# Performance work log

Measured on AMD Instinct MI355X. Metric: run time of the kernel, lower is better.

Reference implementation:

```python
import jax, jax.numpy as jnp
import numpy as np

EPS = 1e-12  # F.normalize eps


def sage_conv(x, src, dst, n_nodes, W_l, b_l, W_r):
    """PyG SAGEConv with mean aggregation and L2 normalize.
    out = lin_l(mean_{j in N(i)} x_j) + lin_r(x_i), then row-wise L2 normalize.
    """
    # mean-aggregate neighbor features: scatter-add then divide by in-degree
    msg_sum = jax.ops.segment_sum(x[src], dst, num_segments=n_nodes)  # [N, F]
    deg = jax.ops.segment_sum(jnp.ones_like(dst, dtype=x.dtype), dst,
                              num_segments=n_nodes)                   # [N]
    agg = msg_sum / jnp.maximum(deg, 1.0)[:, None]
    out = agg @ W_l + b_l + x @ W_r                                   # [N, out]
    norm = jnp.sqrt(jnp.sum(out * out, axis=-1, keepdims=True))
    return out / jnp.maximum(norm, EPS)


def setup_inputs() -> dict:
    key = jax.random.key(0)
    ks = jax.random.split(key, 8)
    N, E, D_IN, D_H, D_OUT = 100000, 320000, 256, 64, 4
    x = jax.random.normal(ks[0], (N, D_IN), dtype=jnp.float32)
    edge_index = jax.random.randint(ks[1], (2, E), 0, N, dtype=jnp.int32)
    s1 = 1.0 / np.sqrt(D_IN)
    s2 = 1.0 / np.sqrt(D_H)
    W1_l = jax.random.uniform(ks[2], (D_IN, D_H), jnp.float32, -s1, s1)
    b1_l = jnp.zeros((D_H,), jnp.float32)
    W1_r = jax.random.uniform(ks[3], (D_IN, D_H), jnp.float32, -s1, s1)
    W2_l = jax.random.uniform(ks[4], (D_H, D_OUT), jnp.float32, -s2, s2)
    b2_l = jnp.zeros((D_OUT,), jnp.float32)
    W2_r = jax.random.uniform(ks[5], (D_H, D_OUT), jnp.float32, -s2, s2)
    return {"x": x, "edge_index": edge_index,
            "W1_l": W1_l, "b1_l": b1_l, "W1_r": W1_r,
            "W2_l": W2_l, "b2_l": b2_l, "W2_r": W2_r}


def reference(x, edge_index, W1_l, b1_l, W1_r, W2_l, b2_l, W2_r):
    # eval mode: dropout is identity
    n_nodes = x.shape[0]
    src, dst = edge_index[0], edge_index[1]
    h = jax.nn.relu(sage_conv(x, src, dst, n_nodes, W1_l, b1_l, W1_r))
    out = sage_conv(h, src, dst, n_nodes, W2_l, b2_l, W2_r)
    return out
```

## Files before the change

### kernel.cpp

```cpp
#include <hip/hip_runtime.h>

#define DIN 256
#define DH  64
#define DOUT 4

typedef __attribute__((ext_vector_type(8))) short bf16x8;
typedef __attribute__((ext_vector_type(4))) float f32x4;

__device__ __forceinline__ short f2bf(float f) {
    unsigned int u = __float_as_uint(f);
    unsigned int r = (u + 0x7FFFu + ((u >> 16) & 1u)) >> 16;
    return (short)r;
}
__device__ __forceinline__ short f2bf_trunc(float f) {
    return (short)(__float_as_uint(f) >> 16);
}
__device__ __forceinline__ float bf2f(short h) {
    return __uint_as_float(((unsigned int)(unsigned short)h) << 16);
}

__global__ void count_kernel(const int* __restrict__ dst, int* __restrict__ cnt, int E) {
    int e = blockIdx.x * blockDim.x + threadIdx.x;
    if (e < E) atomicAdd(&cnt[dst[e]], 1);
}

__global__ void scan_a_kernel(const int* __restrict__ cnt, int* __restrict__ blocksum, int N) {
    __shared__ int s[256];
    const int t = threadIdx.x;
    const int gi = blockIdx.x * 256 + t;
    s[t] = (gi < N) ? cnt[gi] : 0;
    __syncthreads();
    for (int stp = 128; stp > 0; stp >>= 1) {
        if (t < stp) s[t] += s[t + stp];
        __syncthreads();
    }
    if (t == 0) blocksum[blockIdx.x] = s[0];
}

__global__ void scan_b_kernel(int* __restrict__ blocksum, int* __restrict__ blockoff, int nblk) {
    __shared__ int s[1024];
    const int t = threadIdx.x;
    int v = (t < nblk) ? blocksum[t] : 0;
    s[t] = v;
    __syncthreads();
    for (int stp = 1; stp < 1024; stp <<= 1) {
        int add = (t >= stp) ? s[t - stp] : 0;
        __syncthreads();
        s[t] += add;
        __syncthreads();
    }
    if (t < nblk) blockoff[t] = s[t] - v;
}

__global__ void scan_c_kernel(const int* __restrict__ cnt, const int* __restrict__ blockoff,
                              int* __restrict__ off, int N) {
    __shared__ int s[256];
    const int t = threadIdx.x;
    const int gi = blockIdx.x * 256 + t;
    int v = (gi < N) ? cnt[gi] : 0;
    s[t] = v;
    __syncthreads();
    for (int stp = 1; stp < 256; stp <<= 1) {
        int add = (t >= stp) ? s[t - stp] : 0;
        __syncthreads();
        s[t] += add;
        __syncthreads();
    }
    if (gi <= N) off[gi] = blockoff[blockIdx.x] + s[t] - v;
}

__global__ void fill_kernel(const int* __restrict__ src, const int* __restrict__ dst,
                            const int* __restrict__ off, int* __restrict__ cursor,
                            int* __restrict__ nbr, int E) {
    int e = blockIdx.x * blockDim.x + threadIdx.x;
    if (e >= E) return;
    const int d = dst[e];
    const int p = atomicAdd(&cursor[d], 1);
    nbr[off[d] + p] = src[e];
}

__global__ void wprep_kernel(const float* __restrict__ Wl, const float* __restrict__ Wr,
                             short* __restrict__ WTh, short* __restrict__ WTl) {
    const int k = threadIdx.x;
    const int n = blockIdx.x;
    const float v = (n < 64) ? Wl[k * 64 + n] : Wr[k * 64 + (n - 64)];
    const short hi = f2bf(v);
    const short lo = f2bf(v - bf2f(hi));
    WTh[n * 256 + k] = hi;
    WTl[n * 256 + k] = lo;
}

#define XS_LD 40
__global__ __launch_bounds__(256, 4) void gemm1_mfma(
    const float* __restrict__ x, const short* __restrict__ WTh,
    const short* __restrict__ WTl, float* __restrict__ y, int N)
{
    __shared__ short xsh[2][64 * XS_LD];
    __shared__ short xsl[2][64 * XS_LD];

    const int tid  = threadIdx.x;
    const int wave = tid >> 6;
    const int lane = tid & 63;
    const int lm   = lane & 15;
    const int quad = lane >> 4;
    const int brow = blockIdx.x * 64;

    const int xr    = tid >> 2;
    const int xk    = (tid & 3) * 8;
    const int row_g = brow + xr;
    const bool xvalid = (row_g < N);
    const float* xptr = x + (size_t)row_g * DIN + xk;
    const int xs_off = xr * XS_LD + xk;

    const int col0 = wave * 32 + lm;
    const size_t wb0 = (size_t)col0 * 256 + quad * 8;
    const size_t wb1 = (size_t)(col0 + 16) * 256 + quad * 8;

    f32x4 acc[4][2];
    #pragma unroll
    for (int mt = 0; mt < 4; ++mt)
        #pragma unroll
        for (int nt = 0; nt < 2; ++nt)
            acc[mt][nt] = (f32x4){0.f, 0.f, 0.f, 0.f};

    {
        float4 a, b;
        if (xvalid) {
            a = ((const float4*)xptr)[0];
            b = ((const float4*)xptr)[1];
        } else {
            a = b = make_float4(0.f, 0.f, 0.f, 0.f);
        }
        bf16x8 ph, pl;
        float fv[8] = {a.x, a.y, a.z, a.w, b.x, b.y, b.z, b.w};
        #pragma unroll
        for (int j = 0; j < 8; ++j) {
            const short hi = f2bf_trunc(fv[j]);
            ph[j] = hi;
            pl[j] = f2bf_trunc(fv[j] - bf2f(hi));
        }
        *(bf16x8*)(&xsh[0][xs_off]) = ph;
        *(bf16x8*)(&xsl[0][xs_off]) = pl;
    }
    bf16x8 wh_cur[2], wl_cur[2];
    wh_cur[0] = *(const bf16x8*)(WTh + wb0);
    wh_cur[1] = *(const bf16x8*)(WTh + wb1);
    wl_cur[0] = *(const bf16x8*)(WTl + wb0);
    wl_cur[1] = *(const bf16x8*)(WTl + wb1);
    __syncthreads();

    #pragma unroll
    for (int k = 0; k < 8; ++k) {
        const int buf = k & 1;

        float4 na, nb;
        bf16x8 wh_nxt[2], wl_nxt[2];
        if (k < 7) {
            const int kc = (k + 1) * 32;
            if (xvalid) {
                na = ((const float4*)(xptr + kc))[0];
                nb = ((const float4*)(xptr + kc))[1];
            } else {
                na = nb = make_float4(0.f, 0.f, 0.f, 0.f);
            }
            wh_nxt[0] = *(const bf16x8*)(WTh + wb0 + kc);
            wh_nxt[1] = *(const bf16x8*)(WTh + wb1 + kc);
            wl_nxt[0] = *(const bf16x8*)(WTl + wb0 + kc);
            wl_nxt[1] = *(const bf16x8*)(WTl + wb1 + kc);
        }

        #pragma unroll
        for (int mt = 0; mt < 4; ++mt) {
            const int aoff = (mt * 16 + lm) * XS_LD + quad * 8;
            const bf16x8 ah = *(const bf16x8*)(&xsh[buf][aoff]);
            const bf16x8 al = *(const bf16x8*)(&xsl[buf][aoff]);
            #pragma unroll
            for (int nt = 0; nt < 2; ++nt) {
                acc[mt][nt] = __builtin_amdgcn_mfma_f32_16x16x32_bf16(
                    ah, wh_cur[nt], acc[mt][nt], 0, 0, 0);
                acc[mt][nt] = __builtin_amdgcn_mfma_f32_16x16x32_bf16(
                    ah, wl_cur[nt], acc[mt][nt], 0, 0, 0);
                acc[mt][nt] = __builtin_amdgcn_mfma_f32_16x16x32_bf16(
                    al, wh_cur[nt], acc[mt][nt], 0, 0, 0);
            }
        }

        if (k < 7) {
            bf16x8 ph, pl;
            float fv[8] = {na.x, na.y, na.z, na.w, nb.x, nb.y, nb.z, nb.w};
            #pragma unroll
            for (int j = 0; j < 8; ++j) {
                const short hi = f2bf_trunc(fv[j]);
                ph[j] = hi;
                pl[j] = f2bf_trunc(fv[j] - bf2f(hi));
            }
            *(bf16x8*)(&xsh[buf ^ 1][xs_off]) = ph;
            *(bf16x8*)(&xsl[buf ^ 1][xs_off]) = pl;
            #pragma unroll
            for (int nt = 0; nt < 2; ++nt) {
                wh_cur[nt] = wh_nxt[nt];
                wl_cur[nt] = wl_nxt[nt];
            }
            __syncthreads();
        }
    }

    #pragma unroll
    for (int mt = 0; mt < 4; ++mt) {
        #pragma unroll
        for (int r = 0; r < 4; ++r) {
            const int rg = brow + mt * 16 + quad * 4 + r;
            if (rg < N) {
                const int col = wave * 32 + lm;
                float* yp = y + (size_t)rg * 128 + col;
                yp[0]  = acc[mt][0][r];
                yp[16] = acc[mt][1][r];
            }
        }
    }
}

__global__ __launch_bounds__(256) void fused1_kernel(
    const float* __restrict__ y, const int* __restrict__ off, const int* __restrict__ nbr,
    const float* __restrict__ b1, const float* __restrict__ W2l, const float* __restrict__ W2r,
    float* __restrict__ z, int N)
{
    const int wave = threadIdx.x >> 6;
    const int lane = threadIdx.x & 63;
    const int i = blockIdx.x * 4 + wave;
    if (i >= N) return;

    const int beg = off[i];
    const int end = off[i + 1];
    const int deg = end - beg;

    const int dd = (deg < 64) ? deg : 64;
    int myn = (lane < dd) ? nbr[beg + lane] : 0;

    float acc = 0.f;
    int j = 0;
    for (; j + 1 < dd; j += 2) {
        const int s0 = __shfl(myn, j, 64);
        const int s1 = __shfl(myn, j + 1, 64);
        const float v0 = y[(size_t)s0 * 128 + lane];
        const float v1 = y[(size_t)s1 * 128 + lane];
        acc += v0 + v1;
    }
    if (j < dd) {
        const int s0 = __shfl(myn, j, 64);
        acc += y[(size_t)s0 * 128 + lane];
    }
    for (int q = beg + 64; q < end; ++q) {
        const int s = nbr[q];
        acc += y[(size_t)s * 128 + lane];
    }

    const float dinv = 1.0f / fmaxf((float)deg, 1.0f);
    float v = acc * dinv + b1[lane] + y[(size_t)i * 128 + 64 + lane];

    float ss = v * v;
    #pragma unroll
    for (int m = 32; m >= 1; m >>= 1) ss += __shfl_xor(ss, m, 64);
    const float inv = 1.0f / fmaxf(sqrtf(ss), 1e-12f);
    const float hv = fmaxf(v * inv, 0.f);

    const float4 wl = *(const float4*)(W2l + lane * 4);
    const float4 wr = *(const float4*)(W2r + lane * 4);
    float p0 = hv * wl.x, p1 = hv * wl.y, p2 = hv * wl.z, p3 = hv * wl.w;
    float p4 = hv * wr.x, p5 = hv * wr.y, p6 = hv * wr.z, p7 = hv * wr.w;

    const bool b0 = (lane & 1) != 0;
    float s0_ = b0 ? p0 : p4;
    float s1_ = b0 ? p1 : p5;
    float s2_ = b0 ? p2 : p6;
    float s3_ = b0 ? p3 : p7;
    float q0 = (b0 ? p4 : p0) + __shfl_xor(s0_, 1, 64);
    float q1 = (b0 ? p5 : p1) + __shfl_xor(s1_, 1, 64);
    float q2 = (b0 ? p6 : p2) + __shfl_xor(s2_, 1, 64);
    float q3 = (b0 ? p7 : p3) + __shfl_xor(s3_, 1, 64);
    const bool b1b = (lane & 2) != 0;
    float t0 = b1b ? q0 : q2;
    float t1 = b1b ? q1 : q3;
    float r0 = (b1b ? q2 : q0) + __shfl_xor(t0, 2, 64);
    float r1 = (b1b ? q3 : q1) + __shfl_xor(t1, 2, 64);
    const bool b2 = (lane & 4) != 0;
    float u0 = b2 ? r0 : r1;
    float zv = (b2 ? r1 : r0) + __shfl_xor(u0, 4, 64);
    zv += __shfl_xor(zv, 8, 64);
    zv += __shfl_xor(zv, 16, 64);
    zv += __shfl_xor(zv, 32, 64);
    const int ch = 4 * (lane & 1) + ((lane & 2)) + ((lane >> 2) & 1);
    if (lane < 8) z[(size_t)i * 8 + ch] = zv;
}

__global__ void fused2_kernel(const float* __restrict__ z, const int* __restrict__ off,
                              const int* __restrict__ nbr, const float* __restrict__ b2,
                              float* __restrict__ out, int N)
{
    const int i = blockIdx.x * blockDim.x + threadIdx.x;
    if (i >= N) return;
    const int beg = off[i];
    const int end = off[i + 1];
    float4 acc = make_float4(0.f, 0.f, 0.f, 0.f);
    for (int j = beg; j < end; ++j) {
        const int s = nbr[j];
        const float4 t = *(const float4*)(z + (size_t)s * 8);
        acc.x += t.x; acc.y += t.y; acc.z += t.z; acc.w += t.w;
    }
    const float dinv = 1.0f / fmaxf((float)(end - beg), 1.0f);
    const float4 r  = *(const float4*)(z + (size_t)i * 8 + 4);
    const float4 bb = *(const float4*)(b2);
    float4 o;
    o.x = acc.x * dinv + bb.x + r.x;
    o.y = acc.y * dinv + bb.y + r.y;
    o.z = acc.z * dinv + bb.z + r.z;
    o.w = acc.w * dinv + bb.w + r.w;
    const float ss = o.x * o.x + o.y * o.y + o.z * o.z + o.w * o.w;
    const float inv = 1.0f / fmaxf(sqrtf(ss), 1e-12f);
    o.x *= inv; o.y *= inv; o.z *= inv; o.w *= inv;
    *(float4*)(out + (size_t)i * 4) = o;
}

extern "C" void kernel_launch(void* const* d_in, const int* in_sizes, int n_in,
                              void* d_out, int out_size, void* d_ws, size_t ws_size,
                              hipStream_t stream)
{
    const float* x    = (const float*)d_in[0];
    const int*   ei   = (const int*)d_in[1];
    const float* W1l  = (const float*)d_in[2];
    const float* b1l  = (const float*)d_in[3];
    const float* W1r  = (const float*)d_in[4];
    const float* W2l  = (const float*)d_in[5];
    const float* b2l  = (const float*)d_in[6];
    const float* W2r  = (const float*)d_in[7];
    float* out = (float*)d_out;

    const int N = in_sizes[0] / DIN;
    const int E = in_sizes[1] / 2;
    const int* src = ei;
    const int* dst = ei + E;
    const int nblk = (N + 255) / 256;

    char* ws = (char*)d_ws;
    size_t woff = 0;
    auto alloc = [&](size_t bytes) {
        void* p = ws + woff;
        woff += (bytes + 255) & ~(size_t)255;
        return p;
    };
    float* y        = (float*)alloc((size_t)N * 128 * 4);
    float* z        = (float*)alloc((size_t)N * 8 * 4);
    short* WTh      = (short*)alloc((size_t)128 * 256 * 2);
    short* WTl      = (short*)alloc((size_t)128 * 256 * 2);
    int*   cnt      = (int*)alloc((size_t)2 * N * 4);
    int*   cursor   = cnt + N;
    int*   off      = (int*)alloc((size_t)(N + 1) * 4);
    int*   nbr      = (int*)alloc((size_t)E * 4);
    int*   blocksum = (int*)alloc((size_t)nblk * 4);
    int*   blockoff = (int*)alloc((size_t)nblk * 4);

    hipMemsetAsync(cnt, 0, (size_t)2 * N * 4, stream);

    count_kernel<<<(E + 255) / 256, 256, 0, stream>>>(dst, cnt, E);
    scan_a_kernel<<<nblk, 256, 0, stream>>>(cnt, blocksum, N);
    scan_b_kernel<<<1, 1024, 0, stream>>>(blocksum, blockoff, nblk);
    scan_c_kernel<<<nblk, 256, 0, stream>>>(cnt, blockoff, off, N);
    fill_kernel<<<(E + 255) / 256, 256, 0, stream>>>(src, dst, off, cursor, nbr, E);

    wprep_kernel<<<128, 256, 0, stream>>>(W1l, W1r, WTh, WTl);
    gemm1_mfma<<<(N + 63) / 64, 256, 0, stream>>>(x, WTh, WTl, y, N);

    fused1_kernel<<<(N + 3) / 4, 256, 0, stream>>>(y, off, nbr, b1l, W2l, W2r, z, N);

    fused2_kernel<<<(N + 255) / 256, 256, 0, stream>>>(z, off, nbr, b2l, out, N);
}
```

Baseline: 273.8 us.

## Drop LDS staging in GEMM1 and reuse degree counts as fill cursor

The first-layer GEMM no longer stages x tiles through shared memory with block barriers. Each wave now loads its own 32-row strip straight into registers, splits it to bf16 hi/lo, and computes 64 output columns with a two-stage register prefetch of x and weights. This removes the LDS traffic and __syncthreads, but each x row is now read by two waves and register pressure rises, so the occupancy hint drops from 4 to 3. Separately, the CSR fill decrements the count array instead of using a second cursor array, which halves the memset size.

```diff
diff --git a/kernel.cpp b/kernel.cpp
--- a/kernel.cpp
+++ b/kernel.cpp
@@ -70,12 +70,12 @@
 }
 
 __global__ void fill_kernel(const int* __restrict__ src, const int* __restrict__ dst,
-                            const int* __restrict__ off, int* __restrict__ cursor,
+                            const int* __restrict__ off, int* __restrict__ cnt,
                             int* __restrict__ nbr, int E) {
     int e = blockIdx.x * blockDim.x + threadIdx.x;
     if (e >= E) return;
     const int d = dst[e];
-    const int p = atomicAdd(&cursor[d], 1);
+    const int p = atomicSub(&cnt[d], 1) - 1;
     nbr[off[d] + p] = src[e];
 }
 
@@ -90,131 +90,107 @@
     WTl[n * 256 + k] = lo;
 }
 
-#define XS_LD 40
-__global__ __launch_bounds__(256, 4) void gemm1_mfma(
+__global__ __launch_bounds__(256, 3) void gemm1_mfma(
     const float* __restrict__ x, const short* __restrict__ WTh,
     const short* __restrict__ WTl, float* __restrict__ y, int N)
 {
-    __shared__ short xsh[2][64 * XS_LD];
-    __shared__ short xsl[2][64 * XS_LD];
-
-    const int tid  = threadIdx.x;
-    const int wave = tid >> 6;
-    const int lane = tid & 63;
-    const int lm   = lane & 15;
-    const int quad = lane >> 4;
-    const int brow = blockIdx.x * 64;
-
-    const int xr    = tid >> 2;
-    const int xk    = (tid & 3) * 8;
-    const int row_g = brow + xr;
-    const bool xvalid = (row_g < N);
-    const float* xptr = x + (size_t)row_g * DIN + xk;
-    const int xs_off = xr * XS_LD + xk;
-
-    const int col0 = wave * 32 + lm;
-    const size_t wb0 = (size_t)col0 * 256 + quad * 8;
-    const size_t wb1 = (size_t)(col0 + 16) * 256 + quad * 8;
-
-    f32x4 acc[4][2];
-    #pragma unroll
-    for (int mt = 0; mt < 4; ++mt)
+    const int tid   = threadIdx.x;
+    const int wave  = tid >> 6;
+    const int lane  = tid & 63;
+    const int lm    = lane & 15;
+    const int quad  = lane >> 4;
+    const int strip = blockIdx.x * 2 + (wave >> 1);
+    const int ch    = wave & 1;
+    const int wrow  = strip * 32;
+    if (wrow >= N) return;
+
+    const int r0 = min(wrow + lm,      N - 1);
+    const int r1 = min(wrow + 16 + lm, N - 1);
+    const float* xp0 = x + (size_t)r0 * DIN + quad * 8;
+    const float* xp1 = x + (size_t)r1 * DIN + quad * 8;
+
+    const short* wph = WTh + (size_t)(ch * 64 + lm) * 256 + quad * 8;
+    const short* wpl = WTl + (size_t)(ch * 64 + lm) * 256 + quad * 8;
+
+    f32x4 acc[2][4];
+    #pragma unroll
+    for (int mt = 0; mt < 2; ++mt)
         #pragma unroll
-        for (int nt = 0; nt < 2; ++nt)
+        for (int nt = 0; nt < 4; ++nt)
             acc[mt][nt] = (f32x4){0.f, 0.f, 0.f, 0.f};
 
-    {
-        float4 a, b;
-        if (xvalid) {
-            a = ((const float4*)xptr)[0];
-            b = ((const float4*)xptr)[1];
-        } else {
-            a = b = make_float4(0.f, 0.f, 0.f, 0.f);
-        }
-        bf16x8 ph, pl;
-        float fv[8] = {a.x, a.y, a.z, a.w, b.x, b.y, b.z, b.w};
-        #pragma unroll
-        for (int j = 0; j < 8; ++j) {
-            const short hi = f2bf_trunc(fv[j]);
-            ph[j] = hi;
-            pl[j] = f2bf_trunc(fv[j] - bf2f(hi));
-        }
-        *(bf16x8*)(&xsh[0][xs_off]) = ph;
-        *(bf16x8*)(&xsl[0][xs_off]) = pl;
-    }
-    bf16x8 wh_cur[2], wl_cur[2];
-    wh_cur[0] = *(const bf16x8*)(WTh + wb0);
-    wh_cur[1] = *(const bf16x8*)(WTh + wb1);
-    wl_cur[0] = *(const bf16x8*)(WTl + wb0);
-    wl_cur[1] = *(const bf16x8*)(WTl + wb1);
-    __syncthreads();
+    bf16x8 whb[2][4], wlb[2][4];
+    float4 xa[2][2][2];
+
+    xa[0][0][0] = ((const float4*)(xp0))[0];
+    xa[0][0][1] = ((const float4*)(xp0))[1];
+    xa[0][1][0] = ((const float4*)(xp1))[0];
+    xa[0][1][1] = ((const float4*)(xp1))[1];
+    xa[1][0][0] = ((const float4*)(xp0 + 32))[0];
+    xa[1][0][1] = ((const float4*)(xp0 + 32))[1];
+    xa[1][1][0] = ((const float4*)(xp1 + 32))[0];
+    xa[1][1][1] = ((const float4*)(xp1 + 32))[1];
+    #pragma unroll
+    for (int nt = 0; nt < 4; ++nt) {
+        whb[0][nt] = *(const bf16x8*)(wph + nt * 4096);
+        wlb[0][nt] = *(const bf16x8*)(wpl + nt * 4096);
+    }
 
     #pragma unroll
     for (int k = 0; k < 8; ++k) {
-        const int buf = k & 1;
-
-        float4 na, nb;
-        bf16x8 wh_nxt[2], wl_nxt[2];
+        const int s = k & 1;
+
+        bf16x8 ah0, al0, ah1, al1;
+        {
+            float fv0[8] = {xa[s][0][0].x, xa[s][0][0].y, xa[s][0][0].z, xa[s][0][0].w,
+                            xa[s][0][1].x, xa[s][0][1].y, xa[s][0][1].z, xa[s][0][1].w};
+            float fv1[8] = {xa[s][1][0].x, xa[s][1][0].y, xa[s][1][0].z, xa[s][1][0].w,
+                            xa[s][1][1].x, xa[s][1][1].y, xa[s][1][1].z, xa[s][1][1].w};
+            #pragma unroll
+            for (int j = 0; j < 8; ++j) {
+                short h0 = f2bf_trunc(fv0[j]);
+                ah0[j] = h0; al0[j] = f2bf_trunc(fv0[j] - bf2f(h0));
+                short h1 = f2bf_trunc(fv1[j]);
+                ah1[j] = h1; al1[j] = f2bf_trunc(fv1[j] - bf2f(h1));
+            }
+        }
+
+        if (k < 6) {
+            const int kc = (k + 2) * 32;
+            xa[s][0][0] = ((const float4*)(xp0 + kc))[0];
+            xa[s][0][1] = ((const float4*)(xp0 + kc))[1];
+            xa[s][1][0] = ((const float4*)(xp1 + kc))[0];
+            xa[s][1][1] = ((const float4*)(xp1 + kc))[1];
+        }
         if (k < 7) {
             const int kc = (k + 1) * 32;
-            if (xvalid) {
-                na = ((const float4*)(xptr + kc))[0];
-                nb = ((const float4*)(xptr + kc))[1];
-            } else {
-                na = nb = make_float4(0.f, 0.f, 0.f, 0.f);
+            #pragma unroll
+            for (int nt = 0; nt < 4; ++nt) {
+                whb[s ^ 1][nt] = *(const bf16x8*)(wph + nt * 4096 + kc);
+                wlb[s ^ 1][nt] = *(const bf16x8*)(wpl + nt * 4096 + kc);
             }
-            wh_nxt[0] = *(const bf16x8*)(WTh + wb0 + kc);
-            wh_nxt[1] = *(const bf16x8*)(WTh + wb1 + kc);
-            wl_nxt[0] = *(const bf16x8*)(WTl + wb0 + kc);
-            wl_nxt[1] = *(const bf16x8*)(WTl + wb1 + kc);
         }
 
         #pragma unroll
-        for (int mt = 0; mt < 4; ++mt) {
-            const int aoff = (mt * 16 + lm) * XS_LD + quad * 8;
-            const bf16x8 ah = *(const bf16x8*)(&xsh[buf][aoff]);
-            const bf16x8 al = *(const bf16x8*)(&xsl[buf][aoff]);
+        for (int nt = 0; nt < 4; ++nt) {
+            acc[0][nt] = __builtin_amdgcn_mfma_f32_16x16x32_bf16(ah0, whb[s][nt], acc[0][nt], 0, 0, 0);
+            acc[0][nt] = __builtin_amdgcn_mfma_f32_16x16x32_bf16(ah0, wlb[s][nt], acc[0][nt], 0, 0, 0);
+            acc[0][nt] = __builtin_amdgcn_mfma_f32_16x16x32_bf16(al0, whb[s][nt], acc[0][nt], 0, 0, 0);
+            acc[1][nt] = __builtin_amdgcn_mfma_f32_16x16x32_bf16(ah1, whb[s][nt], acc[1][nt], 0, 0, 0);
+            acc[1][nt] = __builtin_amdgcn_mfma_f32_16x16x32_bf16(ah1, wlb[s][nt], acc[1][nt], 0, 0, 0);
+            acc[1][nt] = __builtin_amdgcn_mfma_f32_16x16x32_bf16(al1, whb[s][nt], acc[1][nt], 0, 0, 0);
+        }
+    }
+
+    #pragma unroll
+    for (int mt = 0; mt < 2; ++mt) {
+        #pragma unroll
+        for (int nt = 0; nt < 4; ++nt) {
             #pragma unroll
-            for (int nt = 0; nt < 2; ++nt) {
-                acc[mt][nt] = __builtin_amdgcn_mfma_f32_16x16x32_bf16(
-                    ah, wh_cur[nt], acc[mt][nt], 0, 0, 0);
-                acc[mt][nt] = __builtin_amdgcn_mfma_f32_16x16x32_bf16(
-                    ah, wl_cur[nt], acc[mt][nt], 0, 0, 0);
-                acc[mt][nt] = __builtin_amdgcn_mfma_f32_16x16x32_bf16(
-                    al, wh_cur[nt], acc[mt][nt], 0, 0, 0);
-            }
-        }
-
-        if (k < 7) {
-            bf16x8 ph, pl;
-            float fv[8] = {na.x, na.y, na.z, na.w, nb.x, nb.y, nb.z, nb.w};
-            #pragma unroll
-            for (int j = 0; j < 8; ++j) {
-                const short hi = f2bf_trunc(fv[j]);
-                ph[j] = hi;
-                pl[j] = f2bf_trunc(fv[j] - bf2f(hi));
-            }
-            *(bf16x8*)(&xsh[buf ^ 1][xs_off]) = ph;
-            *(bf16x8*)(&xsl[buf ^ 1][xs_off]) = pl;
-            #pragma unroll
-            for (int nt = 0; nt < 2; ++nt) {
-                wh_cur[nt] = wh_nxt[nt];
-                wl_cur[nt] = wl_nxt[nt];
-            }
-            __syncthreads();
-        }
-    }
-
-    #pragma unroll
-    for (int mt = 0; mt < 4; ++mt) {
-        #pragma unroll
-        for (int r = 0; r < 4; ++r) {
-            const int rg = brow + mt * 16 + quad * 4 + r;
-            if (rg < N) {
-                const int col = wave * 32 + lm;
-                float* yp = y + (size_t)rg * 128 + col;
-                yp[0]  = acc[mt][0][r];
-                yp[16] = acc[mt][1][r];
+            for (int r = 0; r < 4; ++r) {
+                const int rg = wrow + mt * 16 + quad * 4 + r;
+                if (rg < N)
+                    y[(size_t)rg * 128 + ch * 64 + nt * 16 + lm] = acc[mt][nt][r];
             }
         }
     }
@@ -352,23 +328,23 @@
     float* z        = (float*)alloc((size_t)N * 8 * 4);
     short* WTh      = (short*)alloc((size_t)128 * 256 * 2);
     short* WTl      = (short*)alloc((size_t)128 * 256 * 2);
-    int*   cnt      = (int*)alloc((size_t)2 * N * 4);
-    int*   cursor   = cnt + N;
+    int*   cnt      = (int*)alloc((size_t)N * 4);
     int*   off      = (int*)alloc((size_t)(N + 1) * 4);
     int*   nbr      = (int*)alloc((size_t)E * 4);
     int*   blocksum = (int*)alloc((size_t)nblk * 4);
     int*   blockoff = (int*)alloc((size_t)nblk * 4);
 
-    hipMemsetAsync(cnt, 0, (size_t)2 * N * 4, stream);
+    hipMemsetAsync(cnt, 0, (size_t)N * 4, stream);
 
     count_kernel<<<(E + 255) / 256, 256, 0, stream>>>(dst, cnt, E);
     scan_a_kernel<<<nblk, 256, 0, stream>>>(cnt, blocksum, N);
     scan_b_kernel<<<1, 1024, 0, stream>>>(blocksum, blockoff, nblk);
     scan_c_kernel<<<nblk, 256, 0, stream>>>(cnt, blockoff, off, N);
-    fill_kernel<<<(E + 255) / 256, 256, 0, stream>>>(src, dst, off, cursor, nbr, E);
+    fill_kernel<<<(E + 255) / 256, 256, 0, stream>>>(src, dst, off, cnt, nbr, E);
 
     wprep_kernel<<<128, 256, 0, stream>>>(W1l, W1r, WTh, WTl);
-    gemm1_mfma<<<(N + 63) / 64, 256, 0, stream>>>(x, WTh, WTl, y, N);
+    const int nstrips = (N + 31) / 32;
+    gemm1_mfma<<<(nstrips + 1) / 2, 256, 0, stream>>>(x, WTh, WTl, y, N);
 
     fused1_kernel<<<(N + 3) / 4, 256, 0, stream>>>(y, off, nbr, b1l, W2l, W2r, z, N);
 
```

New measurement: 313.5 us. 1.15x slower.
